# Performance work log

Measured on AMD Instinct MI355X. Metric: run time of the kernel, lower is better.

Reference implementation:

```python
import jax, jax.numpy as jnp
import numpy as np

N_NODES = 100000
N_EDGES = 1600000


def spmm(edge_index, edge_vals, x, n_nodes):
    # adj @ x with adj in COO form: out[dst] += val * x[src]
    src = edge_index[0]
    dst = edge_index[1]
    gathered = x[src] * edge_vals[:, None]  # [E, F]
    return jax.ops.segment_sum(gathered, dst, num_segments=n_nodes)


def setup_inputs() -> dict:
    key = jax.random.key(0)
    ks = jax.random.split(key, 8)
    x = jax.random.normal(ks[0], (N_NODES, 512), dtype=jnp.float32)
    edge_index = jax.random.randint(ks[1], (2, N_EDGES), 0, N_NODES, dtype=jnp.int64)
    edge_vals = jax.random.uniform(ks[2], (N_EDGES,), dtype=jnp.float32)
    # xavier-uniform style weights, zero biases (as in initialize_weights)
    def xavier(k, fan_in, fan_out):
        lim = float(np.sqrt(6.0 / (fan_in + fan_out)))
        return jax.random.uniform(k, (fan_in, fan_out), minval=-lim, maxval=lim, dtype=jnp.float32)
    W1 = xavier(ks[3], 512, 128)
    b1 = jnp.zeros((128,), jnp.float32)
    W2 = xavier(ks[4], 128, 64)
    b2 = jnp.zeros((64,), jnp.float32)
    W3 = xavier(ks[5], 64, 16)
    b3 = jnp.zeros((16,), jnp.float32)
    return {"x": x, "edge_index": edge_index, "edge_vals": edge_vals,
            "W1": W1, "b1": b1, "W2": W2, "b2": b2, "W3": W3, "b3": b3}


def reference(x, edge_index, edge_vals, W1, b1, W2, b2, W3, b3):
    n = x.shape[0]
    h = jax.nn.relu(spmm(edge_index, edge_vals, x @ W1 + b1, n))
    h = jax.nn.relu(spmm(edge_index, edge_vals, h @ W2 + b2, n))
    logits = spmm(edge_index, edge_vals, h @ W3 + b3, n)
    logp = jax.nn.log_softmax(logits, axis=1)
    return jnp.argmax(logp, axis=1)
```

## Files before the change

kernel.cpp:

```cpp
#include <hip/hip_runtime.h>

typedef _Float16 half8 __attribute__((ext_vector_type(8)));
typedef float floatx4 __attribute__((ext_vector_type(4)));

__device__ __forceinline__ void g2lds16(const void* g, void* l) {
    __builtin_amdgcn_global_load_lds(
        (const __attribute__((address_space(1))) void*)(unsigned long long)g,
        (__attribute__((address_space(3))) void*)(unsigned int)(unsigned long long)l,
        16, 0, 0);
}


__global__ __launch_bounds__(256) void hist_kernel(const int* __restrict__ dst,
                                                   int* __restrict__ count, int E) {
    int e = blockIdx.x * 256 + threadIdx.x;
    if (e < E) atomicAdd(&count[dst[e]], 1);
}

__global__ __launch_bounds__(1024) void scan_a(const int* __restrict__ count,
                                               int* __restrict__ incl,
                                               int* __restrict__ bsum, int N) {
    __shared__ int s[1024];
    int tid = threadIdx.x;
    int i = blockIdx.x * 1024 + tid;
    int v = (i < N) ? count[i] : 0;
    s[tid] = v;
    __syncthreads();
    for (int off = 1; off < 1024; off <<= 1) {
        int t = (tid >= off) ? s[tid - off] : 0;
        __syncthreads();
        s[tid] += t;
        __syncthreads();
    }
    if (i < N) incl[i] = s[tid];
    if (tid == 1023) bsum[blockIdx.x] = s[1023];
}

__global__ __launch_bounds__(1024) void scan_b(const int* __restrict__ bsum,
                                               int* __restrict__ boff, int NB) {
    __shared__ int s[1024];
    int tid = threadIdx.x;
    int v = (tid < NB) ? bsum[tid] : 0;
    s[tid] = v;
    __syncthreads();
    for (int off = 1; off < 1024; off <<= 1) {
        int t = (tid >= off) ? s[tid - off] : 0;
        __syncthreads();
        s[tid] += t;
        __syncthreads();
    }
    if (tid < NB) boff[tid] = s[tid] - v;
}

__global__ __launch_bounds__(1024) void scan_c(const int* __restrict__ count,
                                               const int* __restrict__ incl,
                                               const int* __restrict__ boff,
                                               int* __restrict__ rowptr,
                                               int* __restrict__ cursor, int N) {
    int i = blockIdx.x * 1024 + threadIdx.x;
    if (i < N) {
        int excl = incl[i] - count[i] + boff[blockIdx.x];
        rowptr[i] = excl;
        cursor[i] = excl;
        if (i == N - 1) rowptr[N] = incl[i] + boff[blockIdx.x];
    }
}

__global__ __launch_bounds__(256) void scatter_kernel(const int* __restrict__ src,
                                                      const int* __restrict__ dst,
                                                      const float* __restrict__ val,
                                                      int* __restrict__ cursor,
                                                      int2* __restrict__ ssv, int E) {
    int e = blockIdx.x * 256 + threadIdx.x;
    if (e < E) {
        int d = dst[e];
        int pos = atomicAdd(&cursor[d], 1);
        int2 p;
        p.x = src[e];
        p.y = __float_as_int(val[e]);
        ssv[pos] = p;
    }
}


__global__ __launch_bounds__(256) void prep_w1(const float* __restrict__ W1,
                                               _Float16* __restrict__ Whi,
                                               _Float16* __restrict__ Wlo) {
    int tid = blockIdx.x * 256 + threadIdx.x;
    int n = tid >> 9;
    int k = tid & 511;
    float w = W1[(size_t)k * 128 + n];
    _Float16 h = (_Float16)w;
    Whi[tid] = h;
    Wlo[tid] = (_Float16)(w - (float)h);
}

__global__ __launch_bounds__(256) void prep_w2(const float* __restrict__ W2,
                                               _Float16* __restrict__ Whi,
                                               _Float16* __restrict__ Wlo) {
    int tid = blockIdx.x * 256 + threadIdx.x;
    int n = tid >> 7;
    int k = tid & 127;
    float w = W2[(size_t)k * 64 + n];
    _Float16 h = (_Float16)w;
    Whi[tid] = h;
    Wlo[tid] = (_Float16)(w - (float)h);
}

__device__ __forceinline__ void split8(float4 f0, float4 f1, half8& h, half8& l) {
    float f[8] = {f0.x, f0.y, f0.z, f0.w, f1.x, f1.y, f1.z, f1.w};
#pragma unroll
    for (int j = 0; j < 8; ++j) {
        _Float16 hi = (_Float16)f[j];
        h[j] = hi;
        l[j] = (_Float16)(f[j] - (float)hi);
    }
}


__global__ __launch_bounds__(256) void gemm1_mfma(const float* __restrict__ X,
                                                  const _Float16* __restrict__ Whi,
                                                  const _Float16* __restrict__ Wlo,
                                                  const float* __restrict__ bias,
                                                  float* __restrict__ out, int M) {
    __shared__ char smem[2 * 16384];
    int t = threadIdx.x;
    int w = t >> 6;
    int lane = t & 63;
    int quad = lane >> 4;
    int l16 = lane & 15;
    int bm = blockIdx.x * 128;
    int m0 = bm + w * 32;

    int ra0 = min(m0 + l16, M - 1);
    int ra1 = min(m0 + 16 + l16, M - 1);
    const float* a0p = X + (size_t)ra0 * 512 + quad * 8;
    const float* a1p = X + (size_t)ra1 * 512 + quad * 8;

    int chunk0 = w * 4;
    const _Float16* gsrc[4];
#pragma unroll
    for (int c = 0; c < 4; ++c) {
        int idx = (chunk0 + c) * 1024 + lane * 16;
        int sec = idx >> 13;
        int row = (idx & 8191) >> 6;
        int kch = (idx >> 4) & 3;
        gsrc[c] = (sec ? Wlo : Whi) + (size_t)row * 512 + kch * 8;
    }
#pragma unroll
    for (int c = 0; c < 4; ++c)
        g2lds16(gsrc[c], smem + (chunk0 + c) * 1024);
    float4 af00 = *(const float4*)(a0p);
    float4 af01 = *(const float4*)(a0p + 4);
    float4 af10 = *(const float4*)(a1p);
    float4 af11 = *(const float4*)(a1p + 4);

    floatx4 acc[2][8];
#pragma unroll
    for (int mt = 0; mt < 2; ++mt)
#pragma unroll
        for (int nt = 0; nt < 8; ++nt) acc[mt][nt] = (floatx4){0.f, 0.f, 0.f, 0.f};

    for (int i = 0; i < 16; ++i) {
        int k0 = i * 32;
        __syncthreads();
        if (i < 15) {
            char* nbuf = smem + ((i + 1) & 1) * 16384;
#pragma unroll
            for (int c = 0; c < 4; ++c)
                g2lds16(gsrc[c] + k0 + 32, nbuf + (chunk0 + c) * 1024);
        }
        float4 nf00 = af00, nf01 = af01, nf10 = af10, nf11 = af11;
        if (i < 15) {
            nf00 = *(const float4*)(a0p + k0 + 32);
            nf01 = *(const float4*)(a0p + k0 + 36);
            nf10 = *(const float4*)(a1p + k0 + 32);
            nf11 = *(const float4*)(a1p + k0 + 36);
        }
        const char* buf = smem + (i & 1) * 16384;
        half8 bh[8], bl[8];
#pragma unroll
        for (int nt = 0; nt < 8; ++nt) {
            int off = (nt * 16 + l16) * 64 + quad * 16;
            bh[nt] = *(const half8*)(buf + off);
            bl[nt] = *(const half8*)(buf + 8192 + off);
        }
        half8 ah0, al0, ah1, al1;
        split8(af00, af01, ah0, al0);
        split8(af10, af11, ah1, al1);
#pragma unroll
        for (int nt = 0; nt < 8; ++nt) {
            acc[0][nt] = __builtin_amdgcn_mfma_f32_16x16x32_f16(ah0, bh[nt], acc[0][nt], 0, 0, 0);
            acc[1][nt] = __builtin_amdgcn_mfma_f32_16x16x32_f16(ah1, bh[nt], acc[1][nt], 0, 0, 0);
            acc[0][nt] = __builtin_amdgcn_mfma_f32_16x16x32_f16(ah0, bl[nt], acc[0][nt], 0, 0, 0);
            acc[1][nt] = __builtin_amdgcn_mfma_f32_16x16x32_f16(ah1, bl[nt], acc[1][nt], 0, 0, 0);
            acc[0][nt] = __builtin_amdgcn_mfma_f32_16x16x32_f16(al0, bh[nt], acc[0][nt], 0, 0, 0);
            acc[1][nt] = __builtin_amdgcn_mfma_f32_16x16x32_f16(al1, bh[nt], acc[1][nt], 0, 0, 0);
        }
        af00 = nf00; af01 = nf01; af10 = nf10; af11 = nf11;
    }

#pragma unroll
    for (int nt = 0; nt < 8; ++nt) {
        int col = nt * 16 + l16;
        float bv = bias[col];
#pragma unroll
        for (int mt = 0; mt < 2; ++mt)
#pragma unroll
            for (int r = 0; r < 4; ++r) {
                int row = m0 + mt * 16 + quad * 4 + r;
                if (row < M) out[(size_t)row * 128 + col] = acc[mt][nt][r] + bv;
            }
    }
}


__global__ __launch_bounds__(256) void gemm2_mfma(const float* __restrict__ H,
                                                  const _Float16* __restrict__ Whi,
                                                  const _Float16* __restrict__ Wlo,
                                                  const float* __restrict__ bias,
                                                  float* __restrict__ out, int M) {
    __shared__ char smem[2 * 64 * 320];
    int t = threadIdx.x;
#pragma unroll
    for (int i = 0; i < 4; ++i) {
        int gidx = i * 256 + t;
        int row = gidx >> 4, col = gidx & 15;
        *(float4*)(smem + row * 320 + col * 16) = ((const float4*)Whi)[gidx];
        *(float4*)(smem + 20480 + row * 320 + col * 16) = ((const float4*)Wlo)[gidx];
    }
    __syncthreads();

    int w = t >> 6;
    int lane = t & 63;
    int quad = lane >> 4;
    int l16 = lane & 15;
    int m0 = blockIdx.x * 128 + w * 32;
    int ra0 = min(m0 + l16, M - 1);
    int ra1 = min(m0 + 16 + l16, M - 1);
    const float* a0p = H + (size_t)ra0 * 128 + quad * 8;
    const float* a1p = H + (size_t)ra1 * 128 + quad * 8;

    floatx4 acc[2][4];
#pragma unroll
    for (int mt = 0; mt < 2; ++mt)
#pragma unroll
        for (int nt = 0; nt < 4; ++nt) acc[mt][nt] = (floatx4){0.f, 0.f, 0.f, 0.f};

#pragma unroll
    for (int k0 = 0; k0 < 128; k0 += 32) {
        float4 af00 = *(const float4*)(a0p + k0);
        float4 af01 = *(const float4*)(a0p + k0 + 4);
        float4 af10 = *(const float4*)(a1p + k0);
        float4 af11 = *(const float4*)(a1p + k0 + 4);
        af00.x = fmaxf(af00.x, 0.f); af00.y = fmaxf(af00.y, 0.f);
        af00.z = fmaxf(af00.z, 0.f); af00.w = fmaxf(af00.w, 0.f);
        af01.x = fmaxf(af01.x, 0.f); af01.y = fmaxf(af01.y, 0.f);
        af01.z = fmaxf(af01.z, 0.f); af01.w = fmaxf(af01.w, 0.f);
        af10.x = fmaxf(af10.x, 0.f); af10.y = fmaxf(af10.y, 0.f);
        af10.z = fmaxf(af10.z, 0.f); af10.w = fmaxf(af10.w, 0.f);
        af11.x = fmaxf(af11.x, 0.f); af11.y = fmaxf(af11.y, 0.f);
        af11.z = fmaxf(af11.z, 0.f); af11.w = fmaxf(af11.w, 0.f);
        half8 bh[4], bl[4];
#pragma unroll
        for (int nt = 0; nt < 4; ++nt) {
            int off = (nt * 16 + l16) * 320 + k0 * 2 + quad * 16;
            bh[nt] = *(const half8*)(smem + off);
            bl[nt] = *(const half8*)(smem + 20480 + off);
        }
        half8 ah0, al0, ah1, al1;
        split8(af00, af01, ah0, al0);
        split8(af10, af11, ah1, al1);
#pragma unroll
        for (int nt = 0; nt < 4; ++nt) {
            acc[0][nt] = __builtin_amdgcn_mfma_f32_16x16x32_f16(ah0, bh[nt], acc[0][nt], 0, 0, 0);
            acc[1][nt] = __builtin_amdgcn_mfma_f32_16x16x32_f16(ah1, bh[nt], acc[1][nt], 0, 0, 0);
            acc[0][nt] = __builtin_amdgcn_mfma_f32_16x16x32_f16(ah0, bl[nt], acc[0][nt], 0, 0, 0);
            acc[1][nt] = __builtin_amdgcn_mfma_f32_16x16x32_f16(ah1, bl[nt], acc[1][nt], 0, 0, 0);
            acc[0][nt] = __builtin_amdgcn_mfma_f32_16x16x32_f16(al0, bh[nt], acc[0][nt], 0, 0, 0);
            acc[1][nt] = __builtin_amdgcn_mfma_f32_16x16x32_f16(al1, bh[nt], acc[1][nt], 0, 0, 0);
        }
    }

#pragma unroll
    for (int nt = 0; nt < 4; ++nt) {
        int col = nt * 16 + l16;
        float bv = bias[col];
#pragma unroll
        for (int mt = 0; mt < 2; ++mt)
#pragma unroll
            for (int r = 0; r < 4; ++r) {
                int row = m0 + mt * 16 + quad * 4 + r;
                if (row < M) out[(size_t)row * 64 + col] = acc[mt][nt][r] + bv;
            }
    }
}


__global__ __launch_bounds__(256) void gemm3(const float* __restrict__ H,
                                             const float* __restrict__ W,
                                             const float* __restrict__ bias,
                                             float* __restrict__ out, int M) {
    __shared__ float Ws[64 * 16];
    __shared__ float Xs[32 * 68];
    int t = threadIdx.x;
    int m0 = blockIdx.x * 32;
    ((float4*)Ws)[t] = ((const float4*)W)[t];
#pragma unroll
    for (int i = 0; i < 2; i++) {
        int idx = t + i * 256;
        int gi = idx * 4;
        int row = gi >> 6, col = gi & 63;
        float4 v = make_float4(0.f, 0.f, 0.f, 0.f);
        if (m0 + row < M) v = *(const float4*)(H + (size_t)(m0 + row) * 64 + col);
        v.x = fmaxf(v.x, 0.f); v.y = fmaxf(v.y, 0.f);
        v.z = fmaxf(v.z, 0.f); v.w = fmaxf(v.w, 0.f);
        *(float4*)&Xs[row * 68 + col] = v;
    }
    __syncthreads();
    int node = t >> 3;
    int j = t & 7;
    float a0 = 0.f, a1 = 0.f;
#pragma unroll 8
    for (int k = 0; k < 64; ++k) {
        float xv = Xs[node * 68 + k];
        a0 += xv * Ws[k * 16 + j * 2];
        a1 += xv * Ws[k * 16 + j * 2 + 1];
    }
    int row = m0 + node;
    if (row < M) {
        a0 += bias[j * 2];
        a1 += bias[j * 2 + 1];
        float2 r = make_float2(a0, a1);
        *(float2*)(out + (size_t)row * 16 + j * 2) = r;
    }
}


__global__ __launch_bounds__(256) void spmm128(const int* __restrict__ rowptr,
                                               const int2* __restrict__ ssv,
                                               const float* __restrict__ T,
                                               float* __restrict__ H, int N) {
    int lane = threadIdx.x & 63;
    int node = __builtin_amdgcn_readfirstlane(blockIdx.x * 4 + (threadIdx.x >> 6));
    if (node >= N) return;
    int beg = rowptr[node], end = rowptr[node + 1];
    float a0 = 0.f, a1 = 0.f;
    int i = beg;
    int n4 = beg + ((end - beg) & ~3);
    for (; i < n4; i += 4) {
        int2 e0 = ssv[i], e1 = ssv[i + 1], e2 = ssv[i + 2], e3 = ssv[i + 3];
        const float* p0 = T + (size_t)e0.x * 128;
        const float* p1 = T + (size_t)e1.x * 128;
        const float* p2 = T + (size_t)e2.x * 128;
        const float* p3 = T + (size_t)e3.x * 128;
        float x0 = p0[lane], y0 = p0[lane + 64];
        float x1 = p1[lane], y1 = p1[lane + 64];
        float x2 = p2[lane], y2 = p2[lane + 64];
        float x3 = p3[lane], y3 = p3[lane + 64];
        float v0 = __int_as_float(e0.y), v1 = __int_as_float(e1.y);
        float v2 = __int_as_float(e2.y), v3 = __int_as_float(e3.y);
        a0 += v0 * x0; a1 += v0 * y0;
        a0 += v1 * x1; a1 += v1 * y1;
        a0 += v2 * x2; a1 += v2 * y2;
        a0 += v3 * x3; a1 += v3 * y3;
    }
    for (; i < end; ++i) {
        int2 e = ssv[i];
        float v = __int_as_float(e.y);
        const float* p = T + (size_t)e.x * 128;
        a0 += v * p[lane];
        a1 += v * p[lane + 64];
    }
    float* o = H + (size_t)node * 128;
    o[lane] = a0;
    o[lane + 64] = a1;
}

__global__ __launch_bounds__(256) void spmm64(const int* __restrict__ rowptr,
                                              const int2* __restrict__ ssv,
                                              const float* __restrict__ T,
                                              float* __restrict__ H, int N) {
    int lane = threadIdx.x & 63;
    int node = __builtin_amdgcn_readfirstlane(blockIdx.x * 4 + (threadIdx.x >> 6));
    if (node >= N) return;
    int beg = rowptr[node], end = rowptr[node + 1];
    float a = 0.f;
    int i = beg;
    int n4 = beg + ((end - beg) & ~3);
    for (; i < n4; i += 4) {
        int2 e0 = ssv[i], e1 = ssv[i + 1], e2 = ssv[i + 2], e3 = ssv[i + 3];
        float x0 = T[(size_t)e0.x * 64 + lane];
        float x1 = T[(size_t)e1.x * 64 + lane];
        float x2 = T[(size_t)e2.x * 64 + lane];
        float x3 = T[(size_t)e3.x * 64 + lane];
        a += __int_as_float(e0.y) * x0;
        a += __int_as_float(e1.y) * x1;
        a += __int_as_float(e2.y) * x2;
        a += __int_as_float(e3.y) * x3;
    }
    for (; i < end; ++i) {
        int2 e = ssv[i];
        a += __int_as_float(e.y) * T[(size_t)e.x * 64 + lane];
    }
    H[(size_t)node * 64 + lane] = a;
}

__global__ __launch_bounds__(256) void spmm_argmax(const int* __restrict__ rowptr,
                                                   const int2* __restrict__ ssv,
                                                   const float* __restrict__ T,
                                                   int* __restrict__ out, int N) {
    int lane = threadIdx.x & 63;
    int wave = threadIdx.x >> 6;
    int sub = lane >> 4;
    int fl = lane & 15;
    int node = blockIdx.x * 16 + wave * 4 + sub;
    float acc = 0.f;
    if (node < N) {
        int beg = rowptr[node], end = rowptr[node + 1];
        int i = beg;
        int n4 = beg + ((end - beg) & ~3);
        for (; i < n4; i += 4) {
            int2 e0 = ssv[i], e1 = ssv[i + 1], e2 = ssv[i + 2], e3 = ssv[i + 3];
            float x0 = T[(size_t)e0.x * 16 + fl];
            float x1 = T[(size_t)e1.x * 16 + fl];
            float x2 = T[(size_t)e2.x * 16 + fl];
            float x3 = T[(size_t)e3.x * 16 + fl];
            acc += __int_as_float(e0.y) * x0;
            acc += __int_as_float(e1.y) * x1;
            acc += __int_as_float(e2.y) * x2;
            acc += __int_as_float(e3.y) * x3;
        }
        for (; i < end; ++i) {
            int2 e = ssv[i];
            acc += __int_as_float(e.y) * T[(size_t)e.x * 16 + fl];
        }
    }
    float bv = acc;
    int bi = fl;
#pragma unroll
    for (int off = 8; off >= 1; off >>= 1) {
        float ov = __shfl_xor(bv, off, 64);
        int oi = __shfl_xor(bi, off, 64);
        if (ov > bv || (ov == bv && oi < bi)) { bv = ov; bi = oi; }
    }
    if (node < N && fl == 0) out[node] = bi;
}


extern "C" void kernel_launch(void* const* d_in, const int* in_sizes, int n_in,
                              void* d_out, int out_size, void* d_ws, size_t ws_size,
                              hipStream_t stream) {
    const float* x  = (const float*)d_in[0];
    const int*   ei = (const int*)d_in[1];
    const float* ev = (const float*)d_in[2];
    const float* W1 = (const float*)d_in[3];
    const float* b1 = (const float*)d_in[4];
    const float* W2 = (const float*)d_in[5];
    const float* b2 = (const float*)d_in[6];
    const float* W3 = (const float*)d_in[7];
    const float* b3 = (const float*)d_in[8];
    int* out = (int*)d_out;

    int M = in_sizes[0] / 512;
    int E = in_sizes[2];
    const int* src = ei;
    const int* dst = ei + E;

    char* ws = (char*)d_ws;
    size_t off = 0;
    auto alloc = [&](size_t bytes) {
        size_t o = off;
        off += (bytes + 255) & ~(size_t)255;
        return o;
    };
    float*    tA     = (float*)(ws + alloc((size_t)M * 128 * 4));
    float*    hB     = (float*)(ws + alloc((size_t)M * 128 * 4));
    int2*     ssv    = (int2*) (ws + alloc((size_t)E * 8));
    int*      rowptr = (int*)  (ws + alloc((size_t)(M + 1) * 4));
    int*      cursor = (int*)  (ws + alloc((size_t)M * 4));
    int*      count  = (int*)  (ws + alloc((size_t)M * 4));
    int*      incl   = (int*)  (ws + alloc((size_t)M * 4));
    int*      bsum   = (int*)  (ws + alloc(4096));
    int*      boff   = (int*)  (ws + alloc(4096));
    _Float16* w1hi   = (_Float16*)(ws + alloc(512 * 128 * 2));
    _Float16* w1lo   = (_Float16*)(ws + alloc(512 * 128 * 2));
    _Float16* w2hi   = (_Float16*)(ws + alloc(128 * 64 * 2));
    _Float16* w2lo   = (_Float16*)(ws + alloc(128 * 64 * 2));

    hipMemsetAsync(count, 0, (size_t)M * 4, stream);
    prep_w1<<<256, 256, 0, stream>>>(W1, w1hi, w1lo);
    prep_w2<<<32, 256, 0, stream>>>(W2, w2hi, w2lo);
    hist_kernel<<<(E + 255) / 256, 256, 0, stream>>>(dst, count, E);
    int NB = (M + 1023) / 1024;
    scan_a<<<NB, 1024, 0, stream>>>(count, incl, bsum, M);
    scan_b<<<1, 1024, 0, stream>>>(bsum, boff, NB);
    scan_c<<<NB, 1024, 0, stream>>>(count, incl, boff, rowptr, cursor, M);
    scatter_kernel<<<(E + 255) / 256, 256, 0, stream>>>(src, dst, ev, cursor, ssv, E);

    gemm1_mfma<<<(M + 127) / 128, 256, 0, stream>>>(x, w1hi, w1lo, b1, tA, M);
    spmm128<<<(M + 3) / 4, 256, 0, stream>>>(rowptr, ssv, tA, hB, M);
    gemm2_mfma<<<(M + 127) / 128, 256, 0, stream>>>(hB, w2hi, w2lo, b2, tA, M);
    spmm64<<<(M + 3) / 4, 256, 0, stream>>>(rowptr, ssv, tA, hB, M);
    gemm3<<<(M + 31) / 32, 256, 0, stream>>>(hB, W3, b3, tA, M);
    spmm_argmax<<<(M + 15) / 16, 256, 0, stream>>>(rowptr, ssv, tA, out, M);
}
```

Measured before the change: 755.3 us.

## Replace global-atomic CSR build with two-pass LDS bucketed counting sort

Replaces the per-edge global-atomic histogram, three-kernel scan and global-atomic scatter with a two-level counting sort. Edges are first binned into 128-node buckets using per-block LDS histograms and LDS cursors, then each bucket is sorted locally in shared memory to produce rowptr and the src/val array. This targets global atomic contention and scattered writes during CSR construction. The cost is extra kernel passes, a temporary buffer aliased onto hB, and packing the in-bucket node index into the high bits of src, which assumes src fits in 20 bits and NBUCK is at most 1024.

```diff
diff --git a/kernel.cpp b/kernel.cpp
--- a/kernel.cpp
+++ b/kernel.cpp
@@ -2,6 +2,11 @@
 
 typedef _Float16 half8 __attribute__((ext_vector_type(8)));
 typedef float floatx4 __attribute__((ext_vector_type(4)));
+
+#define BSHIFT 7
+#define BMASK 127
+#define EPB 8192
+#define P2CAP 4096
 
 __device__ __forceinline__ void g2lds16(const void* g, void* l) {
     __builtin_amdgcn_global_load_lds(
@@ -11,19 +16,44 @@
 }
 
 
-__global__ __launch_bounds__(256) void hist_kernel(const int* __restrict__ dst,
-                                                   int* __restrict__ count, int E) {
-    int e = blockIdx.x * 256 + threadIdx.x;
-    if (e < E) atomicAdd(&count[dst[e]], 1);
-}
-
-__global__ __launch_bounds__(1024) void scan_a(const int* __restrict__ count,
-                                               int* __restrict__ incl,
-                                               int* __restrict__ bsum, int N) {
+__global__ __launch_bounds__(256) void p1a_hist(const int* __restrict__ dst,
+                                                int* __restrict__ hist,
+                                                int E, int NBUCK) {
+    extern __shared__ int lh[];
+    int b = blockIdx.x, t = threadIdx.x;
+    for (int k = t; k < NBUCK; k += 256) lh[k] = 0;
+    __syncthreads();
+    int e0 = b * EPB;
+    int eend = min(e0 + EPB, E);
+    for (int i = e0 + t; i < eend; i += 256)
+        atomicAdd(&lh[dst[i] >> BSHIFT], 1);
+    __syncthreads();
+    for (int k = t; k < NBUCK; k += 256) hist[(size_t)b * NBUCK + k] = lh[k];
+}
+
+__global__ __launch_bounds__(256) void p1b_scan(const int* __restrict__ hist,
+                                                int* __restrict__ blockOff,
+                                                int* __restrict__ btot,
+                                                int NBLK, int NBUCK) {
+    int k = blockIdx.x * 256 + threadIdx.x;
+    if (k < NBUCK) {
+        int run = 0;
+        for (int b = 0; b < NBLK; ++b) {
+            int c = hist[(size_t)b * NBUCK + k];
+            blockOff[(size_t)b * NBUCK + k] = run;
+            run += c;
+        }
+        btot[k] = run;
+    }
+}
+
+__global__ __launch_bounds__(1024) void p1c_bscan(const int* __restrict__ btot,
+                                                  int* __restrict__ bstart,
+                                                  int* __restrict__ rowptr,
+                                                  int NBUCK, int M, int E) {
     __shared__ int s[1024];
     int tid = threadIdx.x;
-    int i = blockIdx.x * 1024 + tid;
-    int v = (i < N) ? count[i] : 0;
+    int v = (tid < NBUCK) ? btot[tid] : 0;
     s[tid] = v;
     __syncthreads();
     for (int off = 1; off < 1024; off <<= 1) {
@@ -32,53 +62,82 @@
         s[tid] += t;
         __syncthreads();
     }
-    if (i < N) incl[i] = s[tid];
-    if (tid == 1023) bsum[blockIdx.x] = s[1023];
-}
-
-__global__ __launch_bounds__(1024) void scan_b(const int* __restrict__ bsum,
-                                               int* __restrict__ boff, int NB) {
-    __shared__ int s[1024];
-    int tid = threadIdx.x;
-    int v = (tid < NB) ? bsum[tid] : 0;
-    s[tid] = v;
-    __syncthreads();
-    for (int off = 1; off < 1024; off <<= 1) {
-        int t = (tid >= off) ? s[tid - off] : 0;
+    if (tid < NBUCK) bstart[tid] = s[tid] - v;
+    if (tid == 0) rowptr[M] = E;
+}
+
+__global__ __launch_bounds__(256) void p1d_scatter(const int* __restrict__ src,
+                                                   const int* __restrict__ dst,
+                                                   const float* __restrict__ val,
+                                                   const int* __restrict__ bstart,
+                                                   const int* __restrict__ blockOff,
+                                                   int2* __restrict__ tmp,
+                                                   int E, int NBUCK) {
+    extern __shared__ int cur[];
+    int b = blockIdx.x, t = threadIdx.x;
+    for (int k = t; k < NBUCK; k += 256)
+        cur[k] = bstart[k] + blockOff[(size_t)b * NBUCK + k];
+    __syncthreads();
+    int e0 = b * EPB;
+    int eend = min(e0 + EPB, E);
+    for (int i = e0 + t; i < eend; i += 256) {
+        int d = dst[i];
+        int p = atomicAdd(&cur[d >> BSHIFT], 1);
+        int2 pk;
+        pk.x = src[i] | ((d & BMASK) << 20);
+        pk.y = __float_as_int(val[i]);
+        tmp[p] = pk;
+    }
+}
+
+__global__ __launch_bounds__(256) void p2_sort(const int2* __restrict__ tmp,
+                                               const int* __restrict__ bstart,
+                                               const int* __restrict__ btot,
+                                               int* __restrict__ rowptr,
+                                               int2* __restrict__ ssv, int M) {
+    __shared__ int2 ebuf[P2CAP];
+    __shared__ int h[128], sc[128], curs[128];
+    int k = blockIdx.x, t = threadIdx.x;
+    int base = bstart[k], n = btot[k];
+    for (int j = t; j < 128; j += 256) h[j] = 0;
+    __syncthreads();
+    int nl = min(n, P2CAP);
+    for (int i = t; i < nl; i += 256) {
+        int2 e = tmp[base + i];
+        ebuf[i] = e;
+        atomicAdd(&h[e.x >> 20], 1);
+    }
+    for (int i = P2CAP + t; i < n; i += 256) {
+        int2 e = tmp[base + i];
+        atomicAdd(&h[e.x >> 20], 1);
+    }
+    __syncthreads();
+    if (t < 128) sc[t] = h[t];
+    __syncthreads();
+    for (int off = 1; off < 128; off <<= 1) {
+        int v = (t < 128 && t >= off) ? sc[t - off] : 0;
         __syncthreads();
-        s[tid] += t;
+        if (t < 128) sc[t] += v;
         __syncthreads();
     }
-    if (tid < NB) boff[tid] = s[tid] - v;
-}
-
-__global__ __launch_bounds__(1024) void scan_c(const int* __restrict__ count,
-                                               const int* __restrict__ incl,
-                                               const int* __restrict__ boff,
-                                               int* __restrict__ rowptr,
-                                               int* __restrict__ cursor, int N) {
-    int i = blockIdx.x * 1024 + threadIdx.x;
-    if (i < N) {
-        int excl = incl[i] - count[i] + boff[blockIdx.x];
-        rowptr[i] = excl;
-        cursor[i] = excl;
-        if (i == N - 1) rowptr[N] = incl[i] + boff[blockIdx.x];
-    }
-}
-
-__global__ __launch_bounds__(256) void scatter_kernel(const int* __restrict__ src,
-                                                      const int* __restrict__ dst,
-                                                      const float* __restrict__ val,
-                                                      int* __restrict__ cursor,
-                                                      int2* __restrict__ ssv, int E) {
-    int e = blockIdx.x * 256 + threadIdx.x;
-    if (e < E) {
-        int d = dst[e];
-        int pos = atomicAdd(&cursor[d], 1);
-        int2 p;
-        p.x = src[e];
-        p.y = __float_as_int(val[e]);
-        ssv[pos] = p;
+    if (t < 128) {
+        int node = (k << BSHIFT) + t;
+        int excl = sc[t] - h[t];
+        if (node < M) rowptr[node] = base + excl;
+        curs[t] = excl;
+    }
+    __syncthreads();
+    for (int i = t; i < nl; i += 256) {
+        int2 e = ebuf[i];
+        int p = atomicAdd(&curs[e.x >> 20], 1);
+        int2 o; o.x = e.x & 0xFFFFF; o.y = e.y;
+        ssv[base + p] = o;
+    }
+    for (int i = P2CAP + t; i < n; i += 256) {
+        int2 e = tmp[base + i];
+        int p = atomicAdd(&curs[e.x >> 20], 1);
+        int2 o; o.x = e.x & 0xFFFFF; o.y = e.y;
+        ssv[base + p] = o;
     }
 }
 
@@ -467,6 +526,9 @@
     const int* src = ei;
     const int* dst = ei + E;
 
+    int NBUCK = (M + BMASK) >> BSHIFT;
+    int NBLK  = (E + EPB - 1) / EPB;
+
     char* ws = (char*)d_ws;
     size_t off = 0;
     auto alloc = [&](size_t bytes) {
@@ -474,29 +536,27 @@
         off += (bytes + 255) & ~(size_t)255;
         return o;
     };
-    float*    tA     = (float*)(ws + alloc((size_t)M * 128 * 4));
-    float*    hB     = (float*)(ws + alloc((size_t)M * 128 * 4));
-    int2*     ssv    = (int2*) (ws + alloc((size_t)E * 8));
-    int*      rowptr = (int*)  (ws + alloc((size_t)(M + 1) * 4));
-    int*      cursor = (int*)  (ws + alloc((size_t)M * 4));
-    int*      count  = (int*)  (ws + alloc((size_t)M * 4));
-    int*      incl   = (int*)  (ws + alloc((size_t)M * 4));
-    int*      bsum   = (int*)  (ws + alloc(4096));
-    int*      boff   = (int*)  (ws + alloc(4096));
-    _Float16* w1hi   = (_Float16*)(ws + alloc(512 * 128 * 2));
-    _Float16* w1lo   = (_Float16*)(ws + alloc(512 * 128 * 2));
-    _Float16* w2hi   = (_Float16*)(ws + alloc(128 * 64 * 2));
-    _Float16* w2lo   = (_Float16*)(ws + alloc(128 * 64 * 2));
-
-    hipMemsetAsync(count, 0, (size_t)M * 4, stream);
+    float*    tA      = (float*)(ws + alloc((size_t)M * 128 * 4));
+    float*    hB      = (float*)(ws + alloc((size_t)M * 128 * 4));
+    int2*     ssv     = (int2*) (ws + alloc((size_t)E * 8));
+    int*      rowptr  = (int*)  (ws + alloc((size_t)(M + 1) * 4));
+    int*      hist    = (int*)  (ws + alloc((size_t)NBLK * NBUCK * 4));
+    int*      blockOff= (int*)  (ws + alloc((size_t)NBLK * NBUCK * 4));
+    int*      btot    = (int*)  (ws + alloc((size_t)NBUCK * 4));
+    int*      bstart  = (int*)  (ws + alloc((size_t)NBUCK * 4));
+    _Float16* w1hi    = (_Float16*)(ws + alloc(512 * 128 * 2));
+    _Float16* w1lo    = (_Float16*)(ws + alloc(512 * 128 * 2));
+    _Float16* w2hi    = (_Float16*)(ws + alloc(128 * 64 * 2));
+    _Float16* w2lo    = (_Float16*)(ws + alloc(128 * 64 * 2));
+    int2*     tmp     = (int2*)hB;
+
     prep_w1<<<256, 256, 0, stream>>>(W1, w1hi, w1lo);
     prep_w2<<<32, 256, 0, stream>>>(W2, w2hi, w2lo);
-    hist_kernel<<<(E + 255) / 256, 256, 0, stream>>>(dst, count, E);
-    int NB = (M + 1023) / 1024;
-    scan_a<<<NB, 1024, 0, stream>>>(count, incl, bsum, M);
-    scan_b<<<1, 1024, 0, stream>>>(bsum, boff, NB);
-    scan_c<<<NB, 1024, 0, stream>>>(count, incl, boff, rowptr, cursor, M);
-    scatter_kernel<<<(E + 255) / 256, 256, 0, stream>>>(src, dst, ev, cursor, ssv, E);
+    p1a_hist<<<NBLK, 256, NBUCK * 4, stream>>>(dst, hist, E, NBUCK);
+    p1b_scan<<<(NBUCK + 255) / 256, 256, 0, stream>>>(hist, blockOff, btot, NBLK, NBUCK);
+    p1c_bscan<<<1, 1024, 0, stream>>>(btot, bstart, rowptr, NBUCK, M, E);
+    p1d_scatter<<<NBLK, 256, NBUCK * 4, stream>>>(src, dst, ev, bstart, blockOff, tmp, E, NBUCK);
+    p2_sort<<<NBUCK, 256, 0, stream>>>(tmp, bstart, btot, rowptr, ssv, M);
 
     gemm1_mfma<<<(M + 127) / 128, 256, 0, stream>>>(x, w1hi, w1lo, b1, tA, M);
     spmm128<<<(M + 3) / 4, 256, 0, stream>>>(rowptr, ssv, tA, hB, M);
```

New measurement: 694.4 us. -8.1%, faster.
